# Performance work log

Hardware: AMD Instinct MI355X
Metric: run time of the kernel (lower is better)

Reference implementation:

```python
import math
import jax, jax.numpy as jnp
import numpy as np

B, T, D = 2, 2048, 1024
NUM_HEADS = 16
NUM_KV_HEADS = 4
HEAD_DIM = 64
ROPE_THETA = 500000.0


def precompute_freqs_cis(dim, seq_len, theta):
    freqs = 1.0 / theta ** (jnp.arange(0, dim, 2).astype(jnp.float32) / dim)
    freqs = jnp.outer(jnp.arange(seq_len), freqs)  # [T, dim//2]
    return jnp.cos(freqs), jnp.sin(freqs)


def apply_rotary_emb(xq, xk, cos, sin):
    # xq:[B,T,H,Dh], cos/sin:[T,Dh//2] -> broadcast as [1,T,1,Dh//2]
    c = cos[None, :, None, :]
    s = sin[None, :, None, :]

    def rot(x):
        xr = x.reshape(*x.shape[:-1], -1, 2)
        x0, x1 = xr[..., 0], xr[..., 1]
        return jnp.stack([x0 * c - x1 * s, x1 * c + x0 * s], axis=-1).reshape(x.shape)

    return rot(xq), rot(xk)


def setup_inputs() -> dict:
    key = jax.random.key(0)
    ks = jax.random.split(key, 5)
    x = jax.random.normal(ks[0], (B, T, D), dtype=jnp.float32)
    # causal mask [B,1,T,T]
    mask = jnp.broadcast_to(jnp.tril(jnp.ones((T, T), dtype=bool))[None, None], (B, 1, T, T))
    sq = 1.0 / math.sqrt(D)
    Wq = jax.random.normal(ks[1], (D, NUM_HEADS * HEAD_DIM), dtype=jnp.float32) * sq
    Wk = jax.random.normal(ks[2], (D, NUM_KV_HEADS * HEAD_DIM), dtype=jnp.float32) * sq
    Wv = jax.random.normal(ks[3], (D, NUM_KV_HEADS * HEAD_DIM), dtype=jnp.float32) * sq
    Wo = jax.random.normal(ks[4], (NUM_HEADS * HEAD_DIM, D), dtype=jnp.float32) * (1.0 / math.sqrt(NUM_HEADS * HEAD_DIM))
    return {"x": x, "mask": mask, "Wq": Wq, "Wk": Wk, "Wv": Wv, "Wo": Wo}


def reference(x, mask, Wq, Wk, Wv, Wo):
    b, t, _ = x.shape
    n_rep = NUM_HEADS // NUM_KV_HEADS
    q = (x @ Wq).reshape(b, t, NUM_HEADS, HEAD_DIM)
    k = (x @ Wk).reshape(b, t, NUM_KV_HEADS, HEAD_DIM)
    v = (x @ Wv).reshape(b, t, NUM_KV_HEADS, HEAD_DIM)
    cos, sin = precompute_freqs_cis(HEAD_DIM, t, ROPE_THETA)
    q, k = apply_rotary_emb(q, k, cos, sin)
    k = jnp.repeat(k, n_rep, axis=2)
    v = jnp.repeat(v, n_rep, axis=2)
    q = q.transpose(0, 2, 1, 3)  # [B,H,T,Dh]
    k = k.transpose(0, 2, 1, 3)
    v = v.transpose(0, 2, 1, 3)
    scale = 1.0 / math.sqrt(HEAD_DIM)
    attn = jnp.einsum('bhqd,bhkd->bhqk', q, k) * scale
    attn = jnp.where(mask, attn, -1e9)
    attn = jax.nn.softmax(attn, axis=-1)
    out = jnp.einsum('bhqk,bhkd->bhqd', attn, v)
    out = out.transpose(0, 2, 1, 3).reshape(b, t, -1)
    return out @ Wo
```

## Files before the change

kernel.cpp:

```cpp
#include <hip/hip_runtime.h>
#include <hip/hip_bf16.h>

#define B_  2
#define T_  2048
#define D_  1024
#define H_  16
#define KH_ 4
#define DH_ 64

typedef __attribute__((ext_vector_type(8))) short bf16x8;
typedef __attribute__((ext_vector_type(4))) float f32x4;

__device__ __forceinline__ unsigned short f2bf(float f) {
  union { float f; unsigned int u; } v; v.f = f;
  return (unsigned short)((v.u + 0x7FFFu + ((v.u >> 16) & 1u)) >> 16);
}
__device__ __forceinline__ unsigned int pack2(float a, float b) {
  return (unsigned int)f2bf(a) | ((unsigned int)f2bf(b) << 16);
}

__global__ __launch_bounds__(256) void prep_kernel(
    const float* __restrict__ x,  const float* __restrict__ Wq,
    const float* __restrict__ Wk, const float* __restrict__ Wv,
    const float* __restrict__ Wo,
    short* __restrict__ xb, short* __restrict__ WT, short* __restrict__ WoT,
    float2* __restrict__ tbl) {
  __shared__ short Ts[64 * 72];
  const int bid = blockIdx.x, tid = threadIdx.x;

  if (bid < 2048) {
    const size_t i8 = ((size_t)bid * 256 + tid) * 8;
    const float4 a = *(const float4*)&x[i8];
    const float4 b = *(const float4*)&x[i8 + 4];
    uint4 p; p.x = pack2(a.x, a.y); p.y = pack2(a.z, a.w);
    p.z = pack2(b.x, b.y); p.w = pack2(b.z, b.w);
    *(uint4*)&xb[i8] = p;
  } else if (bid < 2688) {
    const bool isW = bid < 2432;
    const int idx = isW ? (bid - 2048) : (bid - 2432);
    const int n0 = (idx >> 4) * 64, k0 = (idx & 15) * 64;
    const float* src; int ncols, c0; short* dst;
    if (isW) {
      dst = WT;
      if (n0 < 1024)      { src = Wq; ncols = 1024; c0 = n0; }
      else if (n0 < 1280) { src = Wk; ncols = 256;  c0 = n0 - 1024; }
      else                { src = Wv; ncols = 256;  c0 = n0 - 1280; }
    } else { dst = WoT; src = Wo; ncols = 1024; c0 = n0; }
    for (int i = tid; i < 1024; i += 256) {
      const int kr = i >> 4, c4 = (i & 15) << 2;
      const float4 w = *(const float4*)&src[(size_t)(k0 + kr) * ncols + c0 + c4];
      Ts[(c4 + 0) * 72 + kr] = (short)f2bf(w.x);
      Ts[(c4 + 1) * 72 + kr] = (short)f2bf(w.y);
      Ts[(c4 + 2) * 72 + kr] = (short)f2bf(w.z);
      Ts[(c4 + 3) * 72 + kr] = (short)f2bf(w.w);
    }
    __syncthreads();
    for (int c = tid; c < 512; c += 256) {
      const int nr = c >> 3, c8 = (c & 7) * 8;
      *(bf16x8*)&dst[(size_t)(n0 + nr) * 1024 + k0 + c8] =
          *(const bf16x8*)&Ts[nr * 72 + c8];
    }
  } else {
    const int e = (bid - 2688) * 256 + tid;
    const int t = e >> 5, i2 = e & 31;
    const float freq = exp2f(-(float)(2 * i2) * (18.931568569324174f / 64.0f));
    float sn, cs; sincosf((float)t * freq, &sn, &cs);
    tbl[e] = make_float2(cs, sn);
  }
}

__global__ __launch_bounds__(256) void qkv_mfma_kernel(
    const short* __restrict__ xb, const short* __restrict__ WT,
    const float2* __restrict__ tbl,
    short* __restrict__ qo, short* __restrict__ ko, short* __restrict__ vt) {
  __shared__ short Xs[128 * 72];
  __shared__ short Wt[64 * 72];
  const int tid = threadIdx.x;
  const int lane = tid & 63, w = tid >> 6;
  const int lm = lane & 15, quad = lane >> 4;
  const int m0 = blockIdx.x * 128;
  const int n0 = blockIdx.y * 64;

  f32x4 acc[2][4];
  #pragma unroll
  for (int sm = 0; sm < 2; ++sm)
    #pragma unroll
    for (int ct = 0; ct < 4; ++ct) acc[sm][ct] = (f32x4){0.f, 0.f, 0.f, 0.f};

  bf16x8 px[4], pw[2];
  #pragma unroll
  for (int u = 0; u < 4; ++u) {
    const int c = tid + u * 256, row = c >> 3, c8 = (c & 7) * 8;
    px[u] = *(const bf16x8*)&xb[(size_t)(m0 + row) * 1024 + c8];
  }
  #pragma unroll
  for (int u = 0; u < 2; ++u) {
    const int c = tid + u * 256, row = c >> 3, c8 = (c & 7) * 8;
    pw[u] = *(const bf16x8*)&WT[(size_t)(n0 + row) * 1024 + c8];
  }

  for (int kt = 0; kt < 16; ++kt) {
    __syncthreads();
    #pragma unroll
    for (int u = 0; u < 4; ++u) {
      const int c = tid + u * 256, row = c >> 3, c8 = (c & 7) * 8;
      *(bf16x8*)&Xs[row * 72 + c8] = px[u];
    }
    #pragma unroll
    for (int u = 0; u < 2; ++u) {
      const int c = tid + u * 256, row = c >> 3, c8 = (c & 7) * 8;
      *(bf16x8*)&Wt[row * 72 + c8] = pw[u];
    }
    __syncthreads();
    if (kt < 15) {
      #pragma unroll
      for (int u = 0; u < 4; ++u) {
        const int c = tid + u * 256, row = c >> 3, c8 = (c & 7) * 8;
        px[u] = *(const bf16x8*)&xb[(size_t)(m0 + row) * 1024 + (kt + 1) * 64 + c8];
      }
      #pragma unroll
      for (int u = 0; u < 2; ++u) {
        const int c = tid + u * 256, row = c >> 3, c8 = (c & 7) * 8;
        pw[u] = *(const bf16x8*)&WT[(size_t)(n0 + row) * 1024 + (kt + 1) * 64 + c8];
      }
    }
    #pragma unroll
    for (int s = 0; s < 2; ++s) {
      bf16x8 bfr[4];
      #pragma unroll
      for (int ct = 0; ct < 4; ++ct)
        bfr[ct] = *(const bf16x8*)&Wt[(ct * 16 + lm) * 72 + s * 32 + quad * 8];
      #pragma unroll
      for (int sm = 0; sm < 2; ++sm) {
        const bf16x8 a =
            *(const bf16x8*)&Xs[(w * 32 + sm * 16 + lm) * 72 + s * 32 + quad * 8];
        #pragma unroll
        for (int ct = 0; ct < 4; ++ct)
          acc[sm][ct] =
              __builtin_amdgcn_mfma_f32_16x16x32_bf16(a, bfr[ct], acc[sm][ct], 0, 0, 0);
      }
    }
  }

  if (n0 < 1280) {
    const bool isQ = n0 < 1024;
    short* outp = isQ ? qo : ko;
    const int base = isQ ? n0 : n0 - 1024;
    const int nh = isQ ? H_ : KH_;
    #pragma unroll
    for (int sm = 0; sm < 2; ++sm)
      #pragma unroll
      for (int r = 0; r < 4; ++r) {
        const int row = m0 + w * 32 + sm * 16 + quad * 4 + r;
        const int b = row >> 11, t = row & 2047;
        #pragma unroll
        for (int ct = 0; ct < 4; ++ct) {
          float val = acc[sm][ct][r];
          const float other = __shfl_xor(val, 1);
          const int gc = base + ct * 16 + lm;
          const int ci = gc & 63, hh = gc >> 6;
          const float2 cs = tbl[t * 32 + (ci >> 1)];
          val = ((ci & 1) == 0) ? (val * cs.x - other * cs.y)
                                : (val * cs.x + other * cs.y);
          outp[((size_t)(b * nh + hh) * T_ + t) * DH_ + ci] = (short)f2bf(val);
        }
      }
  } else {
    __syncthreads();
    #pragma unroll
    for (int sm = 0; sm < 2; ++sm)
      #pragma unroll
      for (int r = 0; r < 4; ++r)
        #pragma unroll
        for (int ct = 0; ct < 4; ++ct)
          Xs[(w * 32 + sm * 16 + quad * 4 + r) * 72 + ct * 16 + lm] =
              (short)f2bf(acc[sm][ct][r]);
    __syncthreads();
    const int kh = (n0 - 1280) >> 6;
    const int b = m0 >> 11, t0 = m0 & 2047;
    short* vb = vt + (size_t)(b * KH_ + kh) * DH_ * T_;
    for (int c = tid; c < 1024; c += 256) {
      const int d = c >> 4, c8 = (c & 15) * 8;
      short tmp[8];
      #pragma unroll
      for (int j = 0; j < 8; ++j) tmp[j] = Xs[(c8 + j) * 72 + d];
      *(bf16x8*)&vb[(size_t)d * T_ + t0 + c8] = *(bf16x8*)tmp;
    }
  }
}

__global__ __launch_bounds__(256) void attn_mfma_kernel(
    const short* __restrict__ q, const short* __restrict__ k,
    const short* __restrict__ vt, short* __restrict__ att) {
  __shared__ short Qs[64 * 72];
  __shared__ short Ks[128 * 72];
  __shared__ short Vts[64 * 136];
  __shared__ short Ps[64 * 72];

  const int h = blockIdx.y, b = blockIdx.z;
  const int kh = h >> 2;
  const int tid = threadIdx.x;
  const int lane = tid & 63, w = tid >> 6;
  const int lm = lane & 15, quad = lane >> 4;

  const short* qb = q + (size_t)(b * H_ + h) * T_ * DH_;
  const short* kb = k + (size_t)(b * KH_ + kh) * T_ * DH_;
  const short* vb = vt + (size_t)(b * KH_ + kh) * DH_ * T_;

  bf16x8 ones;
  #pragma unroll
  for (int i = 0; i < 8; ++i) ones[i] = (short)0x3F80;

  const int krow = tid >> 3, kc8 = (tid & 7) * 8;
  const int vd = tid >> 2, vc8 = (tid & 3) * 8;

  for (int half = 0; half < 2; ++half) {
    const int qt = half ? (31 - blockIdx.x) : blockIdx.x;
    const int q0 = qt * 64;

    __syncthreads();
    for (int c = tid; c < 512; c += 256) {
      const int row = c >> 3, c8 = (c & 7) * 8;
      *(bf16x8*)&Qs[row * 72 + c8] =
          *(const bf16x8*)&qb[(size_t)(q0 + row) * 64 + c8];
    }

    f32x4 oacc[4], lacc;
    #pragma unroll
    for (int i = 0; i < 4; ++i) oacc[i] = (f32x4){0.f, 0.f, 0.f, 0.f};
    lacc = (f32x4){0.f, 0.f, 0.f, 0.f};

    bf16x8 pk[4], pv[4];
    #pragma unroll
    for (int u = 0; u < 4; ++u) {
      const int c = tid + u * 256;
      const int row = c >> 3, c8 = (c & 7) * 8;
      pk[u] = *(const bf16x8*)&kb[(size_t)row * 64 + c8];
      const int d = c >> 4, c16 = (c & 15) * 8;
      pv[u] = *(const bf16x8*)&vb[(size_t)d * T_ + c16];
    }

    for (int r2 = 0; r2 <= qt; r2 += 2) {
      __syncthreads();
      #pragma unroll
      for (int u = 0; u < 4; ++u) {
        const int c = tid + u * 256;
        const int row = c >> 3, c8 = (c & 7) * 8;
        *(bf16x8*)&Ks[row * 72 + c8] = pk[u];
        const int d = c >> 4, c16 = (c & 15) * 8;
        *(bf16x8*)&Vts[d * 136 + c16] = pv[u];
      }
      __syncthreads();

      {
        const int r2n = (r2 + 2 <= 30) ? (r2 + 2) : 30;
        #pragma unroll
        for (int u = 0; u < 4; ++u) {
          const int c = tid + u * 256;
          const int row = c >> 3, c8 = (c & 7) * 8;
          pk[u] = *(const bf16x8*)&kb[(size_t)(r2n * 64 + row) * 64 + c8];
          const int d = c >> 4, c16 = (c & 15) * 8;
          pv[u] = *(const bf16x8*)&vb[(size_t)d * T_ + r2n * 64 + c16];
        }
      }

      #pragma unroll
      for (int j = 0; j < 2; ++j) {
        const int kt = r2 + j;
        if (kt > qt) break;

        f32x4 sacc[4];
        #pragma unroll
        for (int i = 0; i < 4; ++i) sacc[i] = (f32x4){0.f, 0.f, 0.f, 0.f};
        #pragma unroll
        for (int s = 0; s < 2; ++s) {
          const bf16x8 a = *(const bf16x8*)&Qs[(w * 16 + lm) * 72 + s * 32 + quad * 8];
          #pragma unroll
          for (int ct = 0; ct < 4; ++ct) {
            const bf16x8 bb =
                *(const bf16x8*)&Ks[(j * 64 + ct * 16 + lm) * 72 + s * 32 + quad * 8];
            sacc[ct] = __builtin_amdgcn_mfma_f32_16x16x32_bf16(a, bb, sacc[ct], 0, 0, 0);
          }
        }

        const bool diag = (kt == qt);
        #pragma unroll
        for (int r = 0; r < 4; ++r) {
          const int qi = w * 16 + quad * 4 + r;
          float p[4];
          #pragma unroll
          for (int ct = 0; ct < 4; ++ct) {
            float pv2 = exp2f(sacc[ct][r] * 0.18033688011112043f);
            if (diag && (ct * 16 + lm) > qi) pv2 = 0.f;
            p[ct] = pv2;
          }
          union { __hip_bfloat162 h2; unsigned int u; } c01, c23;
          c01.h2 = __float22bfloat162_rn(make_float2(p[0], p[1]));
          c23.h2 = __float22bfloat162_rn(make_float2(p[2], p[3]));
          Ps[qi * 72 +      lm] = (short)(c01.u & 0xffffu);
          Ps[qi * 72 + 16 + lm] = (short)(c01.u >> 16);
          Ps[qi * 72 + 32 + lm] = (short)(c23.u & 0xffffu);
          Ps[qi * 72 + 48 + lm] = (short)(c23.u >> 16);
        }
        #pragma unroll
        for (int s = 0; s < 2; ++s) {
          const bf16x8 pa = *(const bf16x8*)&Ps[(w * 16 + lm) * 72 + s * 32 + quad * 8];
          lacc = __builtin_amdgcn_mfma_f32_16x16x32_bf16(pa, ones, lacc, 0, 0, 0);
          #pragma unroll
          for (int ct = 0; ct < 4; ++ct) {
            const bf16x8 vfr = *(const bf16x8*)&Vts[(ct * 16 + lm) * 136 +
                                                    j * 64 + s * 32 + quad * 8];
            oacc[ct] = __builtin_amdgcn_mfma_f32_16x16x32_bf16(pa, vfr, oacc[ct], 0, 0, 0);
          }
        }
      }
    }

    #pragma unroll
    for (int r = 0; r < 4; ++r) {
      const int qrow = q0 + w * 16 + quad * 4 + r;
      const float inv = 1.f / lacc[r];
      #pragma unroll
      for (int ct = 0; ct < 4; ++ct)
        att[((size_t)b * T_ + qrow) * 1024 + h * 64 + ct * 16 + lm] =
            (short)f2bf(oacc[ct][r] * inv);
    }
  }
}

__global__ __launch_bounds__(256) void outproj_mfma_kernel(
    const short* __restrict__ att, const short* __restrict__ WoT,
    float* __restrict__ out) {
  __shared__ short Xs[128 * 72];
  __shared__ short Wt[64 * 72];
  const int tid = threadIdx.x;
  const int lane = tid & 63, w = tid >> 6;
  const int lm = lane & 15, quad = lane >> 4;
  const int m0 = blockIdx.x * 128;
  const int n0 = blockIdx.y * 64;

  f32x4 acc[2][4];
  #pragma unroll
  for (int sm = 0; sm < 2; ++sm)
    #pragma unroll
    for (int ct = 0; ct < 4; ++ct) acc[sm][ct] = (f32x4){0.f, 0.f, 0.f, 0.f};

  bf16x8 px[4], pw[2];
  #pragma unroll
  for (int u = 0; u < 4; ++u) {
    const int c = tid + u * 256, row = c >> 3, c8 = (c & 7) * 8;
    px[u] = *(const bf16x8*)&att[(size_t)(m0 + row) * 1024 + c8];
  }
  #pragma unroll
  for (int u = 0; u < 2; ++u) {
    const int c = tid + u * 256, row = c >> 3, c8 = (c & 7) * 8;
    pw[u] = *(const bf16x8*)&WoT[(size_t)(n0 + row) * 1024 + c8];
  }

  for (int kt = 0; kt < 16; ++kt) {
    __syncthreads();
    #pragma unroll
    for (int u = 0; u < 4; ++u) {
      const int c = tid + u * 256, row = c >> 3, c8 = (c & 7) * 8;
      *(bf16x8*)&Xs[row * 72 + c8] = px[u];
    }
    #pragma unroll
    for (int u = 0; u < 2; ++u) {
      const int c = tid + u * 256, row = c >> 3, c8 = (c & 7) * 8;
      *(bf16x8*)&Wt[row * 72 + c8] = pw[u];
    }
    __syncthreads();
    if (kt < 15) {
      #pragma unroll
      for (int u = 0; u < 4; ++u) {
        const int c = tid + u * 256, row = c >> 3, c8 = (c & 7) * 8;
        px[u] = *(const bf16x8*)&att[(size_t)(m0 + row) * 1024 + (kt + 1) * 64 + c8];
      }
      #pragma unroll
      for (int u = 0; u < 2; ++u) {
        const int c = tid + u * 256, row = c >> 3, c8 = (c & 7) * 8;
        pw[u] = *(const bf16x8*)&WoT[(size_t)(n0 + row) * 1024 + (kt + 1) * 64 + c8];
      }
    }
    #pragma unroll
    for (int s = 0; s < 2; ++s) {
      bf16x8 bfr[4];
      #pragma unroll
      for (int ct = 0; ct < 4; ++ct)
        bfr[ct] = *(const bf16x8*)&Wt[(ct * 16 + lm) * 72 + s * 32 + quad * 8];
      #pragma unroll
      for (int sm = 0; sm < 2; ++sm) {
        const bf16x8 a =
            *(const bf16x8*)&Xs[(w * 32 + sm * 16 + lm) * 72 + s * 32 + quad * 8];
        #pragma unroll
        for (int ct = 0; ct < 4; ++ct)
          acc[sm][ct] =
              __builtin_amdgcn_mfma_f32_16x16x32_bf16(a, bfr[ct], acc[sm][ct], 0, 0, 0);
      }
    }
  }

  #pragma unroll
  for (int sm = 0; sm < 2; ++sm)
    #pragma unroll
    for (int r = 0; r < 4; ++r) {
      const int row = m0 + w * 32 + sm * 16 + quad * 4 + r;
      #pragma unroll
      for (int ct = 0; ct < 4; ++ct)
        out[(size_t)row * 1024 + n0 + ct * 16 + lm] = acc[sm][ct][r];
    }
}

extern "C" void kernel_launch(void* const* d_in, const int* in_sizes, int n_in,
                              void* d_out, int out_size, void* d_ws, size_t ws_size,
                              hipStream_t stream) {
  const float* x  = (const float*)d_in[0];
  const float* Wq = (const float*)d_in[2];
  const float* Wk = (const float*)d_in[3];
  const float* Wv = (const float*)d_in[4];
  const float* Wo = (const float*)d_in[5];
  float* out = (float*)d_out;

  short* xb   = (short*)d_ws;
  short* WT   = xb  + (size_t)4194304;
  short* WoT  = WT  + (size_t)1572864;
  short* qb   = WoT + (size_t)1048576;
  short* kb   = qb  + (size_t)4194304;
  short* vtb  = kb  + (size_t)1048576;
  short* attb = vtb + (size_t)1048576;
  float2* tbl = (float2*)(attb + (size_t)4194304);

  prep_kernel<<<dim3(2944), dim3(256), 0, stream>>>(
      x, Wq, Wk, Wv, Wo, xb, WT, WoT, tbl);
  qkv_mfma_kernel<<<dim3(32, 24), dim3(256), 0, stream>>>(xb, WT, tbl, qb, kb, vtb);
  attn_mfma_kernel<<<dim3(16, H_, B_), dim3(256), 0, stream>>>(qb, kb, vtb, attb);
  outproj_mfma_kernel<<<dim3(32, 16), dim3(256), 0, stream>>>(attb, WoT, out);
}
```

Measured before the change: 189.6 us.

## Launch one attention block per query tile with pre-scaled Q and permuted V

The attention grid now runs one 64-row query tile per block, ordered from the heaviest causal tile to the lightest, instead of pairing two tiles per block. This doubles the number of blocks. The softmax scale is folded into Q in the projection epilogue, so the exp2 no longer needs a multiply. The V transpose writes tokens in a permuted order so each lane's four P values can be stored as one packed 8-byte write in matching column order. Q fragments are hoisted into registers once per block.

```diff
diff --git a/kernel.cpp b/kernel.cpp
--- a/kernel.cpp
+++ b/kernel.cpp
@@ -10,6 +10,8 @@
 
 typedef __attribute__((ext_vector_type(8))) short bf16x8;
 typedef __attribute__((ext_vector_type(4))) float f32x4;
+
+#define QSCALE 0.18033688011112043f
 
 __device__ __forceinline__ unsigned short f2bf(float f) {
   union { float f; unsigned int u; } v; v.f = f;
@@ -147,6 +149,7 @@
     short* outp = isQ ? qo : ko;
     const int base = isQ ? n0 : n0 - 1024;
     const int nh = isQ ? H_ : KH_;
+    const float post = isQ ? QSCALE : 1.0f;
     #pragma unroll
     for (int sm = 0; sm < 2; ++sm)
       #pragma unroll
@@ -162,7 +165,7 @@
           const float2 cs = tbl[t * 32 + (ci >> 1)];
           val = ((ci & 1) == 0) ? (val * cs.x - other * cs.y)
                                 : (val * cs.x + other * cs.y);
-          outp[((size_t)(b * nh + hh) * T_ + t) * DH_ + ci] = (short)f2bf(val);
+          outp[((size_t)(b * nh + hh) * T_ + t) * DH_ + ci] = (short)f2bf(val * post);
         }
       }
   } else {
@@ -183,7 +186,11 @@
       const int d = c >> 4, c8 = (c & 15) * 8;
       short tmp[8];
       #pragma unroll
-      for (int j = 0; j < 8; ++j) tmp[j] = Xs[(c8 + j) * 72 + d];
+      for (int j = 0; j < 8; ++j) {
+        const int s = c8 + j, sg = s & 63;
+        const int tok = (s & 64) + ((sg & 3) << 4) + (sg >> 2);
+        tmp[j] = Xs[tok * 72 + d];
+      }
       *(bf16x8*)&vb[(size_t)d * T_ + t0 + c8] = *(bf16x8*)tmp;
     }
   }
@@ -198,10 +205,12 @@
   __shared__ short Ps[64 * 72];
 
   const int h = blockIdx.y, b = blockIdx.z;
+  const int qt = 31 - blockIdx.x;
   const int kh = h >> 2;
   const int tid = threadIdx.x;
   const int lane = tid & 63, w = tid >> 6;
   const int lm = lane & 15, quad = lane >> 4;
+  const int q0 = qt * 64;
 
   const short* qb = q + (size_t)(b * H_ + h) * T_ * DH_;
   const short* kb = k + (size_t)(b * KH_ + kh) * T_ * DH_;
@@ -211,120 +220,112 @@
   #pragma unroll
   for (int i = 0; i < 8; ++i) ones[i] = (short)0x3F80;
 
-  const int krow = tid >> 3, kc8 = (tid & 7) * 8;
-  const int vd = tid >> 2, vc8 = (tid & 3) * 8;
-
-  for (int half = 0; half < 2; ++half) {
-    const int qt = half ? (31 - blockIdx.x) : blockIdx.x;
-    const int q0 = qt * 64;
-
-    __syncthreads();
-    for (int c = tid; c < 512; c += 256) {
-      const int row = c >> 3, c8 = (c & 7) * 8;
-      *(bf16x8*)&Qs[row * 72 + c8] =
-          *(const bf16x8*)&qb[(size_t)(q0 + row) * 64 + c8];
-    }
-
-    f32x4 oacc[4], lacc;
-    #pragma unroll
-    for (int i = 0; i < 4; ++i) oacc[i] = (f32x4){0.f, 0.f, 0.f, 0.f};
-    lacc = (f32x4){0.f, 0.f, 0.f, 0.f};
-
-    bf16x8 pk[4], pv[4];
+  for (int c = tid; c < 512; c += 256) {
+    const int row = c >> 3, c8 = (c & 7) * 8;
+    *(bf16x8*)&Qs[row * 72 + c8] =
+        *(const bf16x8*)&qb[(size_t)(q0 + row) * 64 + c8];
+  }
+  __syncthreads();
+  bf16x8 aq[2];
+  #pragma unroll
+  for (int s = 0; s < 2; ++s)
+    aq[s] = *(const bf16x8*)&Qs[(w * 16 + lm) * 72 + s * 32 + quad * 8];
+
+  f32x4 oacc[4], lacc;
+  #pragma unroll
+  for (int i = 0; i < 4; ++i) oacc[i] = (f32x4){0.f, 0.f, 0.f, 0.f};
+  lacc = (f32x4){0.f, 0.f, 0.f, 0.f};
+
+  bf16x8 pk[4], pv[4];
+  #pragma unroll
+  for (int u = 0; u < 4; ++u) {
+    const int c = tid + u * 256;
+    const int row = c >> 3, c8 = (c & 7) * 8;
+    pk[u] = *(const bf16x8*)&kb[(size_t)row * 64 + c8];
+    const int d = c >> 4, c16 = (c & 15) * 8;
+    pv[u] = *(const bf16x8*)&vb[(size_t)d * T_ + c16];
+  }
+
+  for (int r2 = 0; r2 <= qt; r2 += 2) {
+    __syncthreads();
     #pragma unroll
     for (int u = 0; u < 4; ++u) {
       const int c = tid + u * 256;
       const int row = c >> 3, c8 = (c & 7) * 8;
-      pk[u] = *(const bf16x8*)&kb[(size_t)row * 64 + c8];
+      *(bf16x8*)&Ks[row * 72 + c8] = pk[u];
       const int d = c >> 4, c16 = (c & 15) * 8;
-      pv[u] = *(const bf16x8*)&vb[(size_t)d * T_ + c16];
-    }
-
-    for (int r2 = 0; r2 <= qt; r2 += 2) {
-      __syncthreads();
+      *(bf16x8*)&Vts[d * 136 + c16] = pv[u];
+    }
+    __syncthreads();
+
+    {
+      const int r2n = (r2 + 2 <= 30) ? (r2 + 2) : 30;
       #pragma unroll
       for (int u = 0; u < 4; ++u) {
         const int c = tid + u * 256;
         const int row = c >> 3, c8 = (c & 7) * 8;
-        *(bf16x8*)&Ks[row * 72 + c8] = pk[u];
+        pk[u] = *(const bf16x8*)&kb[(size_t)(r2n * 64 + row) * 64 + c8];
         const int d = c >> 4, c16 = (c & 15) * 8;
-        *(bf16x8*)&Vts[d * 136 + c16] = pv[u];
-      }
-      __syncthreads();
-
-      {
-        const int r2n = (r2 + 2 <= 30) ? (r2 + 2) : 30;
-        #pragma unroll
-        for (int u = 0; u < 4; ++u) {
-          const int c = tid + u * 256;
-          const int row = c >> 3, c8 = (c & 7) * 8;
-          pk[u] = *(const bf16x8*)&kb[(size_t)(r2n * 64 + row) * 64 + c8];
-          const int d = c >> 4, c16 = (c & 15) * 8;
-          pv[u] = *(const bf16x8*)&vb[(size_t)d * T_ + r2n * 64 + c16];
+        pv[u] = *(const bf16x8*)&vb[(size_t)d * T_ + r2n * 64 + c16];
+      }
+    }
+
+    #pragma unroll
+    for (int j = 0; j < 2; ++j) {
+      const int kt = r2 + j;
+      if (kt > qt) break;
+
+      f32x4 sacc[4];
+      #pragma unroll
+      for (int i = 0; i < 4; ++i) sacc[i] = (f32x4){0.f, 0.f, 0.f, 0.f};
+      #pragma unroll
+      for (int s = 0; s < 2; ++s) {
+        #pragma unroll
+        for (int ct = 0; ct < 4; ++ct) {
+          const bf16x8 bb =
+              *(const bf16x8*)&Ks[(j * 64 + ct * 16 + lm) * 72 + s * 32 + quad * 8];
+          sacc[ct] = __builtin_amdgcn_mfma_f32_16x16x32_bf16(aq[s], bb, sacc[ct], 0, 0, 0);
         }
       }
 
-      #pragma unroll
-      for (int j = 0; j < 2; ++j) {
-        const int kt = r2 + j;
-        if (kt > qt) break;
-
-        f32x4 sacc[4];
-        #pragma unroll
-        for (int i = 0; i < 4; ++i) sacc[i] = (f32x4){0.f, 0.f, 0.f, 0.f};
-        #pragma unroll
-        for (int s = 0; s < 2; ++s) {
-          const bf16x8 a = *(const bf16x8*)&Qs[(w * 16 + lm) * 72 + s * 32 + quad * 8];
-          #pragma unroll
-          for (int ct = 0; ct < 4; ++ct) {
-            const bf16x8 bb =
-                *(const bf16x8*)&Ks[(j * 64 + ct * 16 + lm) * 72 + s * 32 + quad * 8];
-            sacc[ct] = __builtin_amdgcn_mfma_f32_16x16x32_bf16(a, bb, sacc[ct], 0, 0, 0);
-          }
+      const bool diag = (kt == qt);
+      #pragma unroll
+      for (int r = 0; r < 4; ++r) {
+        const int qi = w * 16 + quad * 4 + r;
+        float p[4];
+        #pragma unroll
+        for (int ct = 0; ct < 4; ++ct) {
+          float pv2 = exp2f(sacc[ct][r]);
+          if (diag && (ct * 16 + lm) > qi) pv2 = 0.f;
+          p[ct] = pv2;
         }
-
-        const bool diag = (kt == qt);
-        #pragma unroll
-        for (int r = 0; r < 4; ++r) {
-          const int qi = w * 16 + quad * 4 + r;
-          float p[4];
-          #pragma unroll
-          for (int ct = 0; ct < 4; ++ct) {
-            float pv2 = exp2f(sacc[ct][r] * 0.18033688011112043f);
-            if (diag && (ct * 16 + lm) > qi) pv2 = 0.f;
-            p[ct] = pv2;
-          }
-          union { __hip_bfloat162 h2; unsigned int u; } c01, c23;
-          c01.h2 = __float22bfloat162_rn(make_float2(p[0], p[1]));
-          c23.h2 = __float22bfloat162_rn(make_float2(p[2], p[3]));
-          Ps[qi * 72 +      lm] = (short)(c01.u & 0xffffu);
-          Ps[qi * 72 + 16 + lm] = (short)(c01.u >> 16);
-          Ps[qi * 72 + 32 + lm] = (short)(c23.u & 0xffffu);
-          Ps[qi * 72 + 48 + lm] = (short)(c23.u >> 16);
+        uint2 pk2;
+        pk2.x = pack2(p[0], p[1]);
+        pk2.y = pack2(p[2], p[3]);
+        *(uint2*)&Ps[qi * 72 + lm * 4] = pk2;
+      }
+      #pragma unroll
+      for (int s = 0; s < 2; ++s) {
+        const bf16x8 pa = *(const bf16x8*)&Ps[(w * 16 + lm) * 72 + s * 32 + quad * 8];
+        lacc = __builtin_amdgcn_mfma_f32_16x16x32_bf16(pa, ones, lacc, 0, 0, 0);
+        #pragma unroll
+        for (int ct = 0; ct < 4; ++ct) {
+          const bf16x8 vfr = *(const bf16x8*)&Vts[(ct * 16 + lm) * 136 +
+                                                  j * 64 + s * 32 + quad * 8];
+          oacc[ct] = __builtin_amdgcn_mfma_f32_16x16x32_bf16(pa, vfr, oacc[ct], 0, 0, 0);
         }
-        #pragma unroll
-        for (int s = 0; s < 2; ++s) {
-          const bf16x8 pa = *(const bf16x8*)&Ps[(w * 16 + lm) * 72 + s * 32 + quad * 8];
-          lacc = __builtin_amdgcn_mfma_f32_16x16x32_bf16(pa, ones, lacc, 0, 0, 0);
-          #pragma unroll
-          for (int ct = 0; ct < 4; ++ct) {
-            const bf16x8 vfr = *(const bf16x8*)&Vts[(ct * 16 + lm) * 136 +
-                                                    j * 64 + s * 32 + quad * 8];
-            oacc[ct] = __builtin_amdgcn_mfma_f32_16x16x32_bf16(pa, vfr, oacc[ct], 0, 0, 0);
-          }
-        }
-      }
-    }
-
-    #pragma unroll
-    for (int r = 0; r < 4; ++r) {
-      const int qrow = q0 + w * 16 + quad * 4 + r;
-      const float inv = 1.f / lacc[r];
-      #pragma unroll
-      for (int ct = 0; ct < 4; ++ct)
-        att[((size_t)b * T_ + qrow) * 1024 + h * 64 + ct * 16 + lm] =
-            (short)f2bf(oacc[ct][r] * inv);
-    }
+      }
+    }
+  }
+
+  #pragma unroll
+  for (int r = 0; r < 4; ++r) {
+    const int qrow = q0 + w * 16 + quad * 4 + r;
+    const float inv = 1.f / lacc[r];
+    #pragma unroll
+    for (int ct = 0; ct < 4; ++ct)
+      att[((size_t)b * T_ + qrow) * 1024 + h * 64 + ct * 16 + lm] =
+          (short)f2bf(oacc[ct][r] * inv);
   }
 }
 
@@ -433,6 +434,6 @@
   prep_kernel<<<dim3(2944), dim3(256), 0, stream>>>(
       x, Wq, Wk, Wv, Wo, xb, WT, WoT, tbl);
   qkv_mfma_kernel<<<dim3(32, 24), dim3(256), 0, stream>>>(xb, WT, tbl, qb, kb, vtb);
-  attn_mfma_kernel<<<dim3(16, H_, B_), dim3(256), 0, stream>>>(qb, kb, vtb, attb);
+  attn_mfma_kernel<<<dim3(32, H_, B_), dim3(256), 0, stream>>>(qb, kb, vtb, attb);
   outproj_mfma_kernel<<<dim3(32, 16), dim3(256), 0, stream>>>(attb, WoT, out);
 }
```

New measurement: 219.8 us. 1.16x slower.
